# Kernel optimization log

Hardware: AMD Instinct MI355X
Metric: run time of the kernel (lower is better)

The kernel has to match this reference:

```python
import jax, jax.numpy as jnp
import numpy as np

ALPHA = 4.0          # spikingjelly default surrogate.Sigmoid(alpha=4.0)
V_TH = 1.0           # IFNode default v_threshold
BN_EPS = 1e-5

@jax.custom_vjp
def spike(x):
    # heaviside forward
    return (x >= 0.0).astype(x.dtype)

def _spike_fwd(x):
    return spike(x), x

def _spike_bwd(x, g):
    s = jax.nn.sigmoid(ALPHA * x)
    return (g * ALPHA * s * (1.0 - s),)

spike.defvjp(_spike_fwd, _spike_bwd)

def if_node(x_seq):
    """Multi-step IF neuron: integrate, threshold, hard reset (v_reset=0),
    detach_reset=True. x_seq: [T, ...] -> spikes [T, ...]."""
    def step(v, xt):
        v = v + xt
        s = spike(v - V_TH)
        v = v * (1.0 - jax.lax.stop_gradient(s))  # detached hard reset to 0
        return v, s
    _, s_seq = jax.lax.scan(step, jnp.zeros_like(x_seq[0]), x_seq)
    return s_seq

def bn1d(x, gamma, beta):
    """Training-mode BatchNorm1d over flattened (T*B) batch dim. x: [T,B,F]."""
    m = x.mean(axis=(0, 1))
    v = x.var(axis=(0, 1))  # biased variance, matches torch normalization
    return (x - m) * jax.lax.rsqrt(v + BN_EPS) * gamma + beta

def setup_inputs() -> dict:
    key = jax.random.key(0)
    ks = jax.random.split(key, 12)
    T, B, C, H, W = 8, 64, 2, 128, 128
    F0, D, NC = C * H * W, 2048, 1000
    x = jax.random.uniform(ks[0], (T, B, C, H, W), dtype=jnp.float32)
    def kaiming(k, out_f, in_f):
        # kaiming_normal_ mode='fan_out', relu gain: std = sqrt(2/out_f)
        return jax.random.normal(k, (out_f, in_f), dtype=jnp.float32) * np.sqrt(2.0 / out_f)
    def bias(k, out_f, in_f):
        bound = 1.0 / np.sqrt(in_f)
        return jax.random.uniform(k, (out_f,), dtype=jnp.float32, minval=-bound, maxval=bound)
    inp = {"x": x}
    dims = [(D, F0), (D, D), (D, D)]
    for i, (o, f) in enumerate(dims):
        inp[f"W{i}"] = kaiming(ks[1 + i], o, f)
        inp[f"b{i}"] = bias(ks[4 + i], o, f)
        inp[f"g{i}"] = jnp.ones((o,), jnp.float32)
        inp[f"be{i}"] = jnp.zeros((o,), jnp.float32)
    inp["Wout"] = kaiming(ks[7], NC, D)
    inp["bout"] = bias(ks[8], NC, D)
    return inp

def reference(x, W0, b0, g0, be0, W1, b1, g1, be1, W2, b2, g2, be2, Wout, bout):
    T, B = x.shape[0], x.shape[1]
    h = x.reshape(T, B, -1)           # [T,B,32768]
    h = if_node(h)                    # sn0
    for Wl, bl, gl, bel in ((W0, b0, g0, be0), (W1, b1, g1, be1), (W2, b2, g2, be2)):
        h = jnp.einsum('tbi,oi->tbo', h, Wl) + bl
        h = bn1d(h, gl, bel)
        h = if_node(h)
    out = jnp.einsum('tbi,oi->tbo', h, Wout) + bout  # [T,B,1000]
    return out.mean(axis=0)           # [B,1000]
```

## Files before the change

### kernel.cpp

```cpp
#include <hip/hip_runtime.h>


#define T_STEPS 8
#define BATCH 64
#define F0 32768
#define DIM 2048
#define NROWS 512
#define NC 1000

typedef __attribute__((ext_vector_type(8))) short short8;
typedef __attribute__((ext_vector_type(4))) float f32x4;

__device__ __forceinline__ unsigned short bf16_rne(float f) {
    unsigned int u = __float_as_uint(f);
    u += 0x7FFFu + ((u >> 16) & 1u);
    return (unsigned short)(u >> 16);
}

#define BM 128
#define BN 128
#define BK 64

__device__ __forceinline__ short8 lds_frag(const unsigned short* base, int row, int kb) {
    const int off = row * 128 + (kb ^ ((row & 7) << 4));
    return *(const short8*)((const char*)base + off);
}

__global__ __launch_bounds__(256) void gemm_splitk(
    const unsigned short* __restrict__ A, const float* __restrict__ W,
    float* __restrict__ part, int M, int N, int K, int Kpart, int Wrows)
{
    __shared__ unsigned short As[BM * BK];
    __shared__ unsigned short Hs[BN * BK];
    __shared__ unsigned short Ls[BN * BK];

    const int tid  = threadIdx.x;
    const int lane = tid & 63;
    const int w    = tid >> 6;
    const int bm   = blockIdx.x * BM;
    const int bn   = blockIdx.y * BN;
    const int kz   = blockIdx.z;
    const int ksteps = Kpart / BK;

    const int wm = (w >> 1) * 64;
    const int wn = (w & 1) * 64;

    f32x4 acc[4][4] = {};

    for (int kt = 0; kt < ksteps; ++kt) {
        const int k0 = kz * Kpart + kt * BK;

#pragma unroll
        for (int c = 0; c < 4; ++c) {
            const int r    = w * 32 + c * 8 + (lane >> 3);
            const int colb = ((lane & 7) * 16) ^ ((r & 7) << 4);
            const char* src = (const char*)A + ((size_t)(bm + r) * K + k0) * 2 + colb;
            unsigned short* dst = &As[(w * 32 + c * 8) * BK];
            __builtin_amdgcn_global_load_lds(
                (const __attribute__((address_space(1))) void*)src,
                (__attribute__((address_space(3))) void*)dst, 16, 0, 0);
        }

        float4 wv[8];
#pragma unroll
        for (int i = 0; i < 8; ++i) {
            const int q  = tid + 256 * i;
            const int n  = q >> 4;
            const int c4 = q & 15;
            const int gn = min(bn + n, Wrows - 1);
            wv[i] = *(const float4*)&W[(size_t)gn * K + k0 + c4 * 4];
        }
#pragma unroll
        for (int i = 0; i < 8; ++i) {
            const int q  = tid + 256 * i;
            const int n  = q >> 4;
            const int c4 = q & 15;
            const float vf[4] = {wv[i].x, wv[i].y, wv[i].z, wv[i].w};
            unsigned short h[4], l[4];
#pragma unroll
            for (int e = 0; e < 4; ++e) {
                h[e] = bf16_rne(vf[e]);
                const float hf = __uint_as_float((unsigned int)h[e] << 16);
                l[e] = bf16_rne(vf[e] - hf);
            }
            const int off = n * 128 + (((c4 * 8)) ^ ((n & 7) << 4));
            *(ushort4*)((char*)Hs + off) = make_ushort4(h[0], h[1], h[2], h[3]);
            *(ushort4*)((char*)Ls + off) = make_ushort4(l[0], l[1], l[2], l[3]);
        }

        __syncthreads();

#pragma unroll
        for (int kk = 0; kk < 2; ++kk) {
            const int kb = (kk * 32 + (lane >> 4) * 8) * 2;
            short8 a[4], bh[4], bl[4];
#pragma unroll
            for (int i = 0; i < 4; ++i)
                a[i] = lds_frag(As, wm + i * 16 + (lane & 15), kb);
#pragma unroll
            for (int i = 0; i < 4; ++i) {
                const int r = wn + i * 16 + (lane & 15);
                bh[i] = lds_frag(Hs, r, kb);
                bl[i] = lds_frag(Ls, r, kb);
            }
#pragma unroll
            for (int mi = 0; mi < 4; ++mi)
#pragma unroll
                for (int ni = 0; ni < 4; ++ni) {
                    acc[mi][ni] = __builtin_amdgcn_mfma_f32_16x16x32_bf16(
                        a[mi], bh[ni], acc[mi][ni], 0, 0, 0);
                    acc[mi][ni] = __builtin_amdgcn_mfma_f32_16x16x32_bf16(
                        a[mi], bl[ni], acc[mi][ni], 0, 0, 0);
                }
        }
        __syncthreads();
    }

    const size_t zoff = (size_t)kz * M * N;
#pragma unroll
    for (int mi = 0; mi < 4; ++mi) {
        const int gr0 = bm + wm + mi * 16 + (lane >> 4) * 4;
#pragma unroll
        for (int ni = 0; ni < 4; ++ni) {
            const int gc = bn + wn + ni * 16 + (lane & 15);
            if (gc < N) {
#pragma unroll
                for (int e = 0; e < 4; ++e) {
                    const int gr = gr0 + e;
                    if (gr < M) part[zoff + (size_t)gr * N + gc] = acc[mi][ni][e];
                }
            }
        }
    }
}

__global__ __launch_bounds__(256) void reduce_bias(
    const float* __restrict__ part, const float* __restrict__ bias,
    float* __restrict__ out, int KS, int MN, int N)
{
    const int i4 = blockIdx.x * 256 + threadIdx.x;
    if (i4 * 4 >= MN) return;
    float4 s = make_float4(0.f, 0.f, 0.f, 0.f);
    for (int z = 0; z < KS; ++z) {
        const float4 p = *(const float4*)&part[(size_t)z * MN + i4 * 4];
        s.x += p.x; s.y += p.y; s.z += p.z; s.w += p.w;
    }
    const int col = (i4 * 4) % N;
    const float4 b = *(const float4*)&bias[col];
    s.x += b.x; s.y += b.y; s.z += b.z; s.w += b.w;
    *(float4*)&out[(size_t)i4 * 4] = s;
}

__global__ __launch_bounds__(256) void if0_kernel(
    const float* __restrict__ x, unsigned short* __restrict__ s)
{
    const size_t id = (size_t)blockIdx.x * blockDim.x + threadIdx.x;
    float v = 0.f;
#pragma unroll
    for (int t = 0; t < T_STEPS; ++t) {
        const size_t idx = (size_t)t * (BATCH * (size_t)F0) + id;
        v += x[idx];
        if (v >= 1.0f) { s[idx] = 0x3F80; v = 0.f; }
        else           { s[idx] = 0; }
    }
}

__global__ __launch_bounds__(256) void bn_stats(
    const float* __restrict__ z, const float* __restrict__ g,
    const float* __restrict__ be, float* __restrict__ scale,
    float* __restrict__ shift)
{
    __shared__ float ssum[4][64], ssq[4][64];
    const int l = threadIdx.x & 63;
    const int q = threadIdx.x >> 6;
    const int f = blockIdx.x * 64 + l;
    float sum = 0.f, sq = 0.f;
    for (int r = q; r < NROWS; r += 4) {
        const float v = z[(size_t)r * DIM + f];
        sum += v; sq += v * v;
    }
    ssum[q][l] = sum; ssq[q][l] = sq;
    __syncthreads();
    if (threadIdx.x < 64) {
        float ts = 0.f, tq = 0.f;
#pragma unroll
        for (int i = 0; i < 4; ++i) { ts += ssum[i][l]; tq += ssq[i][l]; }
        const float mean = ts * (1.0f / NROWS);
        const float var  = tq * (1.0f / NROWS) - mean * mean;
        const float inv  = rsqrtf(var + 1e-5f);
        const float sc   = g[f] * inv;
        scale[f] = sc;
        shift[f] = be[f] - mean * sc;
    }
}

__global__ __launch_bounds__(256) void bn_if(
    const float* __restrict__ z, const float* __restrict__ scale,
    const float* __restrict__ shift, unsigned short* __restrict__ s)
{
    const int id = blockIdx.x * blockDim.x + threadIdx.x;
    const int o  = id & (DIM - 1);
    const float sc = scale[o];
    const float sh = shift[o];
    float v = 0.f;
#pragma unroll
    for (int t = 0; t < T_STEPS; ++t) {
        const size_t idx = (size_t)t * (BATCH * DIM) + id;
        v += z[idx] * sc + sh;
        if (v >= 1.0f) { s[idx] = 0x3F80; v = 0.f; }
        else           { s[idx] = 0; }
    }
}

__global__ __launch_bounds__(256) void sbar_kernel(
    const unsigned short* __restrict__ s3, unsigned short* __restrict__ sbar)
{
    const int id = blockIdx.x * blockDim.x + threadIdx.x;
    int cnt = 0;
#pragma unroll
    for (int t = 0; t < T_STEPS; ++t)
        cnt += (s3[(size_t)t * (BATCH * DIM) + id] >> 7) & 1;
    sbar[id] = bf16_rne((float)cnt * 0.125f);
}

extern "C" void kernel_launch(void* const* d_in, const int* in_sizes, int n_in,
                              void* d_out, int out_size, void* d_ws, size_t ws_size,
                              hipStream_t stream)
{
    const float* x    = (const float*)d_in[0];
    const float* W0   = (const float*)d_in[1];
    const float* b0   = (const float*)d_in[2];
    const float* g0   = (const float*)d_in[3];
    const float* be0  = (const float*)d_in[4];
    const float* W1   = (const float*)d_in[5];
    const float* b1   = (const float*)d_in[6];
    const float* g1   = (const float*)d_in[7];
    const float* be1  = (const float*)d_in[8];
    const float* W2   = (const float*)d_in[9];
    const float* b2   = (const float*)d_in[10];
    const float* g2   = (const float*)d_in[11];
    const float* be2  = (const float*)d_in[12];
    const float* Wout = (const float*)d_in[13];
    const float* bout = (const float*)d_in[14];
    float* out = (float*)d_out;
    (void)in_sizes; (void)n_in; (void)out_size; (void)ws_size;

    char* ws = (char*)d_ws;
    size_t off = 0;
    auto alloc = [&](size_t nbytes) {
        char* p = ws + off;
        off = (off + nbytes + 255) & ~(size_t)255;
        return p;
    };
    unsigned short* s0 = (unsigned short*)alloc((size_t)NROWS * F0 * 2);
    unsigned short* s1 = (unsigned short*)alloc((size_t)NROWS * DIM * 2);
    unsigned short* s2 = (unsigned short*)alloc((size_t)NROWS * DIM * 2);
    unsigned short* s3 = (unsigned short*)alloc((size_t)NROWS * DIM * 2);
    unsigned short* sb = (unsigned short*)alloc((size_t)128 * DIM * 2);
    float* z    = (float*)alloc((size_t)NROWS * DIM * 4);
    float* part = (float*)alloc((size_t)8 * NROWS * DIM * 4);
    float* scale = (float*)alloc(DIM * 4);
    float* shift = (float*)alloc(DIM * 4);

    const int MN = NROWS * DIM;

    if0_kernel<<<(BATCH * (size_t)F0) / 256, 256, 0, stream>>>(x, s0);

    gemm_splitk<<<dim3(NROWS / BM, DIM / BN, 8), 256, 0, stream>>>(
        s0, W0, part, NROWS, DIM, F0, F0 / 8, DIM);
    reduce_bias<<<MN / 4 / 256, 256, 0, stream>>>(part, b0, z, 8, MN, DIM);
    bn_stats<<<DIM / 64, 256, 0, stream>>>(z, g0, be0, scale, shift);
    bn_if<<<(BATCH * DIM) / 256, 256, 0, stream>>>(z, scale, shift, s1);

    gemm_splitk<<<dim3(NROWS / BM, DIM / BN, 4), 256, 0, stream>>>(
        s1, W1, part, NROWS, DIM, DIM, DIM / 4, DIM);
    reduce_bias<<<MN / 4 / 256, 256, 0, stream>>>(part, b1, z, 4, MN, DIM);
    bn_stats<<<DIM / 64, 256, 0, stream>>>(z, g1, be1, scale, shift);
    bn_if<<<(BATCH * DIM) / 256, 256, 0, stream>>>(z, scale, shift, s2);

    gemm_splitk<<<dim3(NROWS / BM, DIM / BN, 4), 256, 0, stream>>>(
        s2, W2, part, NROWS, DIM, DIM, DIM / 4, DIM);
    reduce_bias<<<MN / 4 / 256, 256, 0, stream>>>(part, b2, z, 4, MN, DIM);
    bn_stats<<<DIM / 64, 256, 0, stream>>>(z, g2, be2, scale, shift);
    bn_if<<<(BATCH * DIM) / 256, 256, 0, stream>>>(z, scale, shift, s3);

    sbar_kernel<<<(BATCH * DIM) / 256, 256, 0, stream>>>(s3, sb);
    gemm_splitk<<<dim3(1, (NC + BN - 1) / BN, 4), 256, 0, stream>>>(
        sb, Wout, part, BATCH, NC, DIM, DIM / 4, NC);
    reduce_bias<<<(BATCH * NC / 4 + 255) / 256, 256, 0, stream>>>(
        part, bout, out, 4, BATCH * NC, NC);
}
```

Measured before the change: 429.1 us.

## Remap GEMM workgroups across XCDs, raise split-K factors, fuse final IF with time-mean

```diff
diff --git a/kernel.cpp b/kernel.cpp
--- a/kernel.cpp
+++ b/kernel.cpp
@@ -34,12 +34,20 @@
     __shared__ unsigned short Hs[BN * BK];
     __shared__ unsigned short Ls[BN * BK];
 
+    const int gx = gridDim.x, gy = gridDim.y;
+    const int nwg = gx * gy * gridDim.z;
+    const int lid = blockIdx.x + gx * (blockIdx.y + gy * blockIdx.z);
+    const int cpx = nwg >> 3;
+    const int nid = (lid & 7) * cpx + (lid >> 3);
+    const int bx  = nid % gx;
+    const int by  = (nid / gx) % gy;
+    const int kz  = nid / (gx * gy);
+
     const int tid  = threadIdx.x;
     const int lane = tid & 63;
     const int w    = tid >> 6;
-    const int bm   = blockIdx.x * BM;
-    const int bn   = blockIdx.y * BN;
-    const int kz   = blockIdx.z;
+    const int bm   = bx * BM;
+    const int bn   = by * BN;
     const int ksteps = Kpart / BK;
 
     const int wm = (w >> 1) * 64;
@@ -212,14 +220,22 @@
     }
 }
 
-__global__ __launch_bounds__(256) void sbar_kernel(
-    const unsigned short* __restrict__ s3, unsigned short* __restrict__ sbar)
+__global__ __launch_bounds__(256) void bn_if_mean(
+    const float* __restrict__ z, const float* __restrict__ scale,
+    const float* __restrict__ shift, unsigned short* __restrict__ sbar)
 {
     const int id = blockIdx.x * blockDim.x + threadIdx.x;
+    const int o  = id & (DIM - 1);
+    const float sc = scale[o];
+    const float sh = shift[o];
+    float v = 0.f;
     int cnt = 0;
 #pragma unroll
-    for (int t = 0; t < T_STEPS; ++t)
-        cnt += (s3[(size_t)t * (BATCH * DIM) + id] >> 7) & 1;
+    for (int t = 0; t < T_STEPS; ++t) {
+        const size_t idx = (size_t)t * (BATCH * DIM) + id;
+        v += z[idx] * sc + sh;
+        if (v >= 1.0f) { cnt++; v = 0.f; }
+    }
     sbar[id] = bf16_rne((float)cnt * 0.125f);
 }
 
@@ -255,10 +271,9 @@
     unsigned short* s0 = (unsigned short*)alloc((size_t)NROWS * F0 * 2);
     unsigned short* s1 = (unsigned short*)alloc((size_t)NROWS * DIM * 2);
     unsigned short* s2 = (unsigned short*)alloc((size_t)NROWS * DIM * 2);
-    unsigned short* s3 = (unsigned short*)alloc((size_t)NROWS * DIM * 2);
     unsigned short* sb = (unsigned short*)alloc((size_t)128 * DIM * 2);
     float* z    = (float*)alloc((size_t)NROWS * DIM * 4);
-    float* part = (float*)alloc((size_t)8 * NROWS * DIM * 4);
+    float* part = (float*)alloc((size_t)16 * NROWS * DIM * 4);
     float* scale = (float*)alloc(DIM * 4);
     float* shift = (float*)alloc(DIM * 4);
 
@@ -266,25 +281,24 @@
 
     if0_kernel<<<(BATCH * (size_t)F0) / 256, 256, 0, stream>>>(x, s0);
 
-    gemm_splitk<<<dim3(NROWS / BM, DIM / BN, 8), 256, 0, stream>>>(
-        s0, W0, part, NROWS, DIM, F0, F0 / 8, DIM);
-    reduce_bias<<<MN / 4 / 256, 256, 0, stream>>>(part, b0, z, 8, MN, DIM);
+    gemm_splitk<<<dim3(NROWS / BM, DIM / BN, 16), 256, 0, stream>>>(
+        s0, W0, part, NROWS, DIM, F0, F0 / 16, DIM);
+    reduce_bias<<<MN / 4 / 256, 256, 0, stream>>>(part, b0, z, 16, MN, DIM);
     bn_stats<<<DIM / 64, 256, 0, stream>>>(z, g0, be0, scale, shift);
     bn_if<<<(BATCH * DIM) / 256, 256, 0, stream>>>(z, scale, shift, s1);
 
-    gemm_splitk<<<dim3(NROWS / BM, DIM / BN, 4), 256, 0, stream>>>(
-        s1, W1, part, NROWS, DIM, DIM, DIM / 4, DIM);
-    reduce_bias<<<MN / 4 / 256, 256, 0, stream>>>(part, b1, z, 4, MN, DIM);
+    gemm_splitk<<<dim3(NROWS / BM, DIM / BN, 8), 256, 0, stream>>>(
+        s1, W1, part, NROWS, DIM, DIM, DIM / 8, DIM);
+    reduce_bias<<<MN / 4 / 256, 256, 0, stream>>>(part, b1, z, 8, MN, DIM);
     bn_stats<<<DIM / 64, 256, 0, stream>>>(z, g1, be1, scale, shift);
     bn_if<<<(BATCH * DIM) / 256, 256, 0, stream>>>(z, scale, shift, s2);
 
-    gemm_splitk<<<dim3(NROWS / BM, DIM / BN, 4), 256, 0, stream>>>(
-        s2, W2, part, NROWS, DIM, DIM, DIM / 4, DIM);
-    reduce_bias<<<MN / 4 / 256, 256, 0, stream>>>(part, b2, z, 4, MN, DIM);
+    gemm_splitk<<<dim3(NROWS / BM, DIM / BN, 8), 256, 0, stream>>>(
+        s2, W2, part, NROWS, DIM, DIM, DIM / 8, DIM);
+    reduce_bias<<<MN / 4 / 256, 256, 0, stream>>>(part, b2, z, 8, MN, DIM);
     bn_stats<<<DIM / 64, 256, 0, stream>>>(z, g2, be2, scale, shift);
-    bn_if<<<(BATCH * DIM) / 256, 256, 0, stream>>>(z, scale, shift, s3);
-
-    sbar_kernel<<<(BATCH * DIM) / 256, 256, 0, stream>>>(s3, sb);
+    bn_if_mean<<<(BATCH * DIM) / 256, 256, 0, stream>>>(z, scale, shift, sb);
+
     gemm_splitk<<<dim3(1, (NC + BN - 1) / BN, 4), 256, 0, stream>>>(
         sb, Wout, part, BATCH, NC, DIM, DIM / 4, NC);
     reduce_bias<<<(BATCH * NC / 4 + 255) / 256, 256, 0, stream>>>(
```

After: 408.4 us. 1.05x faster.
